# Kernel tuning notes

Measured on AMD Instinct MI355X. Metric: run time of the kernel, lower is better.

The kernel has to match this reference:

```python
import jax, jax.numpy as jnp
import numpy as np

N, B, M, K, C = 120000, 8, 60000, 16, 32
EX = 512  # 128 * expansion_factor 4
EPS = 1e-5


def _bn(h, g, b):
    # BatchNorm1d (training-mode batch stats, biased var), stats over points
    m = h.mean(axis=0)
    v = h.var(axis=0)
    return (h - m) * jax.lax.rsqrt(v + EPS) * g + b


def setup_inputs() -> dict:
    key = jax.random.key(0)
    ks = jax.random.split(key, 20)

    def w(i, shape, fan):
        return jax.random.normal(ks[i], shape, jnp.float32) / np.sqrt(fan)

    inp = {}
    inp["x"] = jax.random.normal(ks[0], (N, C), jnp.float32)
    inp["pos"] = jax.random.normal(ks[1], (N, 3), jnp.float32) * 5.0
    inp["batch"] = jnp.sort(jax.random.randint(ks[2], (N,), 0, B))
    inp["reflectance"] = jax.random.uniform(ks[3], (N,), jnp.float32)
    inp["sf"] = jax.random.uniform(ks[4], (B,), jnp.float32, minval=0.5, maxval=1.5)
    inp["idx"] = jnp.sort(jax.random.randint(ks[5], (M,), 0, N))
    inp["edge_src"] = jax.random.randint(ks[6], (M * K,), 0, N)
    inp["edge_dst"] = jnp.repeat(jnp.arange(M), K)
    # local_nn MLP channels [C+4, 64, 64, 128]; first layer has no BN
    inp["mlp_W1"] = w(7, (C + 4, 64), C + 4); inp["mlp_b1"] = jnp.zeros((64,))
    inp["mlp_W2"] = w(8, (64, 64), 64); inp["mlp_b2"] = jnp.zeros((64,))
    inp["mlp_g2"] = jnp.ones((64,)); inp["mlp_be2"] = jnp.zeros((64,))
    inp["mlp_W3"] = w(9, (64, 128), 64); inp["mlp_b3"] = jnp.zeros((128,))
    inp["mlp_g3"] = jnp.ones((128,)); inp["mlp_be3"] = jnp.zeros((128,))
    # ReflectanceYesNo (1 -> 32 -> 32 -> 1)
    inp["ryn_W1"] = w(10, (1, 32), 1); inp["ryn_b1"] = jnp.zeros((32,))
    inp["ryn_W2"] = w(11, (32, 32), 32); inp["ryn_b2"] = jnp.zeros((32,))
    inp["ryn_W3"] = w(12, (32, 1), 32); inp["ryn_b3"] = jnp.zeros((1,))
    # InvertedResidualBlock 128 -> 512 -> 128 (all 1x1 convs)
    inp["exp_W"] = w(13, (128, EX), 128); inp["exp_b"] = jnp.zeros((EX,))
    inp["exp_g"] = jnp.ones((EX,)); inp["exp_be"] = jnp.zeros((EX,))
    inp["dw_w"] = jax.random.normal(ks[14], (2, EX), jnp.float32)  # depthwise k=1 -> per-channel scale
    inp["dw_b"] = jnp.zeros((2, EX)); inp["dw_g"] = jnp.ones((2, EX)); inp["dw_be"] = jnp.zeros((2, EX))
    inp["pw_W"] = w(15, (2, EX, EX), EX); inp["pw_b"] = jnp.zeros((2, EX))
    inp["pw_g"] = jnp.ones((2, EX)); inp["pw_be"] = jnp.zeros((2, EX))
    inp["c_g"] = jnp.ones((2, EX)); inp["c_be"] = jnp.zeros((2, EX))
    inp["proj_W"] = w(16, (EX, 128), EX); inp["proj_b"] = jnp.zeros((128,))
    inp["proj_g"] = jnp.ones((128,)); inp["proj_be"] = jnp.zeros((128,))
    return inp


def reference(x, pos, batch, reflectance, sf, idx, edge_src, edge_dst,
              mlp_W1, mlp_b1, mlp_W2, mlp_b2, mlp_g2, mlp_be2, mlp_W3, mlp_b3, mlp_g3, mlp_be3,
              ryn_W1, ryn_b1, ryn_W2, ryn_b2, ryn_W3, ryn_b3,
              exp_W, exp_b, exp_g, exp_be, dw_w, dw_b, dw_g, dw_be,
              pw_W, pw_b, pw_g, pw_be, c_g, c_be, proj_W, proj_b, proj_g, proj_be):
    Bn = sf.shape[0]
    Mn = idx.shape[0]
    pos4 = jnp.concatenate([pos[:, :3], reflectance[:, None]], axis=-1)  # [N,4]

    # --- ReflectanceYesNo gating (gumbel_softmax over a size-1 axis == ones, straight-through) ---
    h = jax.nn.relu(reflectance[:, None] @ ryn_W1 + ryn_b1)
    h = jax.nn.relu(h @ ryn_W2 + ryn_b2)
    pooled = jax.ops.segment_sum(h, batch, num_segments=Bn)
    counts = jax.ops.segment_sum(jnp.ones((h.shape[0],), h.dtype), batch, num_segments=Bn)
    logits = (pooled / counts[:, None]) @ ryn_W3 + ryn_b3  # [B,1]
    y_soft = jax.nn.softmax(logits, axis=-1)               # size-1 softmax -> all ones
    y = jax.lax.stop_gradient(jnp.ones_like(y_soft) - y_soft) + y_soft
    gate = jnp.where(jnp.sum(reflectance) != 0.0, y[:, 0][batch], 1.0)
    refl4 = pos4[:, 3] * gate

    # --- scale coords, PointNetConv: gather -> local_nn MLP -> max aggregate ---
    scale = sf[batch][:, None]
    pos_s = jnp.concatenate([pos4[:, :3] / scale, refl4[:, None]], axis=-1)  # [N,4]
    rel = pos_s[edge_src] - pos_s[idx][edge_dst]                              # [E,4]
    msg = jnp.concatenate([x[edge_src], rel], axis=-1)                        # [E,C+4]
    h1 = jax.nn.relu(msg @ mlp_W1 + mlp_b1)
    h2 = _bn(jax.nn.relu(h1 @ mlp_W2 + mlp_b2), mlp_g2, mlp_be2)
    h3 = _bn(jax.nn.relu(h2 @ mlp_W3 + mlp_b3), mlp_g3, mlp_be3)
    agg = jax.ops.segment_max(h3, edge_dst, num_segments=Mn)                  # [M,128]
    agg = jnp.where(jnp.isneginf(agg), 0.0, agg)  # PyG fills isolated nodes with 0

    # --- InvertedResidualBlock (1x1 convs == per-point linears, BN over points) ---
    res = agg
    e = jax.nn.relu(_bn(agg @ exp_W + exp_b, exp_g, exp_be))

    def ds(hh, i):  # DepthwiseSeparableConv1d, k=1
        d = jax.nn.relu(_bn(hh * dw_w[i] + dw_b[i], dw_g[i], dw_be[i]))
        return jax.nn.relu(_bn(d @ pw_W[i] + pw_b[i], pw_g[i], pw_be[i]))

    cmid = jax.nn.relu(_bn(ds(e, 0), c_g[0], c_be[0]))
    cmid = _bn(ds(cmid, 1), c_g[1], c_be[1])
    o = _bn(cmid @ proj_W + proj_b, proj_g, proj_be)
    out = jax.nn.relu(o + res)  # shortcut is identity (in == out channels)

    return (out, pos[idx, :3], batch[idx], reflectance[idx], sf)
```

## Files before the change

### kernel.cpp

```cpp
#include <hip/hip_runtime.h>
#include <hip/hip_bf16.h>
#include <cstdint>

#define DEV_INLINE __device__ __forceinline__

typedef unsigned short u16;
typedef unsigned int   u32;
typedef short bf16x8 __attribute__((ext_vector_type(8)));
typedef float f32x4  __attribute__((ext_vector_type(4)));

constexpr int NP = 120000, NB = 8, NM = 60000, KNN = 16;
constexpr int NE = NM * KNN;
constexpr float EPS = 1e-5f;

constexpr size_t O_POS   = (size_t)NM * 128;
constexpr size_t O_BATCH = O_POS + (size_t)NM * 3;
constexpr size_t O_REFL  = O_BATCH + NM;
constexpr size_t O_SF    = O_REFL + NM;

__device__ float  g_pos_s[(size_t)NP * 4];
__device__ u16    g_xbf[(size_t)NP * 32];
__device__ u16    g_pre2[(size_t)NE * 64];
__device__ u32    g_mm[(size_t)NM * 128];
__device__ float  g_agg[(size_t)NM * 128];
__device__ u16    g_aggbf[(size_t)NM * 128];
__device__ u16    g_bufA[(size_t)NM * 512];
__device__ u16    g_bufB[(size_t)NM * 512];
__device__ float  g_obuf[(size_t)NM * 128];
__device__ float  g_sum[512], g_sqs[512], g_cfa[512], g_cfb[512];
__device__ float  g_b3adj[128], g_pbadj[128];
__device__ u16 g_w1t[64 * 64];
__device__ u16 g_w2t[64 * 64];
__device__ u16 g_w3t[128 * 64];
__device__ u16 g_expwt[512 * 128];
__device__ u16 g_pw0t[512 * 512];
__device__ u16 g_pw1t[512 * 512];
__device__ u16 g_projwt[128 * 512];

template<int ID> DEV_INLINE const u16* ubufsel() {
  if constexpr (ID == 1) return g_aggbf;
  else if constexpr (ID == 2) return g_bufA;
  else return g_bufB;
}
template<int ID> DEV_INLINE u16* obufsel() {
  if constexpr (ID == 2) return g_bufA;
  else return g_bufB;
}
template<int ID> DEV_INLINE const u16* wsel() {
  if constexpr (ID == 3) return g_expwt;
  else if constexpr (ID == 4) return g_pw0t;
  else if constexpr (ID == 5) return g_pw1t;
  else return g_projwt;
}

DEV_INLINE float bf2f(u16 u) { u32 x = (u32)u << 16; float f; __builtin_memcpy(&f, &x, 4); return f; }
DEV_INLINE u16 f2bf(float f) {
  u32 x; __builtin_memcpy(&x, &f, 4);
  return (u16)((x + 0x7FFFu + ((x >> 16) & 1u)) >> 16);
}
DEV_INLINE u32 pack2(float a, float b) { return (u32)f2bf(a) | ((u32)f2bf(b) << 16); }

DEV_INLINE uint4 affine8(uint4 v, int kbase, bool relu) {
  u32 u[4] = {v.x, v.y, v.z, v.w};
  u32 r[4];
#pragma unroll
  for (int q = 0; q < 4; q++) {
    float lo = bf2f((u16)(u[q] & 0xFFFFu));
    float hi = bf2f((u16)(u[q] >> 16));
    lo = fmaf(g_cfa[kbase + 2*q],     lo, g_cfb[kbase + 2*q]);
    hi = fmaf(g_cfa[kbase + 2*q + 1], hi, g_cfb[kbase + 2*q + 1]);
    if (relu) { lo = fmaxf(lo, 0.f); hi = fmaxf(hi, 0.f); }
    r[q] = (u32)f2bf(lo) | ((u32)f2bf(hi) << 16);
  }
  return make_uint4(r[0], r[1], r[2], r[3]);
}

__global__ void prep_pos_x(const float* __restrict__ pos, const int* __restrict__ batch,
                           const float* __restrict__ refl, const float* __restrict__ sf,
                           const float* __restrict__ x) {
  int i = blockIdx.x * blockDim.x + threadIdx.x;
  if (i >= NP) return;
  float s = sf[batch[i]];
  float4 v;
  v.x = pos[(size_t)i*3+0] / s;
  v.y = pos[(size_t)i*3+1] / s;
  v.z = pos[(size_t)i*3+2] / s;
  v.w = refl[i];
  *reinterpret_cast<float4*>(g_pos_s + (size_t)i*4) = v;
  const float4* xr = reinterpret_cast<const float4*>(x + (size_t)i*32);
#pragma unroll
  for (int q = 0; q < 4; q++) {
    float4 a = xr[q*2], b = xr[q*2+1];
    uint4 u = make_uint4(pack2(a.x,a.y), pack2(a.z,a.w), pack2(b.x,b.y), pack2(b.z,b.w));
    *reinterpret_cast<uint4*>(g_xbf + (size_t)i*32 + q*8) = u;
  }
}

__global__ void tail_out(const float* __restrict__ pos, const int* __restrict__ batch,
                         const float* __restrict__ refl, const float* __restrict__ sf,
                         const int* __restrict__ idx, float* __restrict__ out) {
  int i = blockIdx.x * blockDim.x + threadIdx.x;
  if (i < NM) {
    int p = idx[i];
    out[O_POS + (size_t)i*3+0] = pos[(size_t)p*3+0];
    out[O_POS + (size_t)i*3+1] = pos[(size_t)p*3+1];
    out[O_POS + (size_t)i*3+2] = pos[(size_t)p*3+2];
    out[O_BATCH + i] = (float)batch[p];
    out[O_REFL  + i] = refl[p];
  }
  if (i < NB) out[O_SF + i] = sf[i];
}

__global__ void zero_stats() {
  int t = threadIdx.x;
  g_sum[t] = 0.f; g_sqs[t] = 0.f;
}

__global__ void prep_weights(const float* __restrict__ W1, const float* __restrict__ W2,
                             const float* __restrict__ W3, const float* __restrict__ expW,
                             const float* __restrict__ pwW, const float* __restrict__ projW) {
  int i = blockIdx.x * 256 + threadIdx.x;
  const int s0 = 4096, s1 = 4096, s2 = 8192, s3 = 65536, s4 = 262144, s5 = 262144, s6 = 65536;
  if (i < s0) { int n = i >> 6, k = i & 63; g_w1t[i] = (k < 36) ? f2bf(W1[k*64 + n]) : (u16)0; return; }
  i -= s0;
  if (i < s1) { int n = i >> 6, k = i & 63; g_w2t[i] = f2bf(W2[k*64 + n]); return; }
  i -= s1;
  if (i < s2) { int n = i >> 6, k = i & 63; g_w3t[i] = f2bf(W3[k*128 + n]); return; }
  i -= s2;
  if (i < s3) { int n = i >> 7, k = i & 127; g_expwt[i] = f2bf(expW[k*512 + n]); return; }
  i -= s3;
  if (i < s4) { int n = i >> 9, k = i & 511; g_pw0t[i] = f2bf(pwW[k*512 + n]); return; }
  i -= s4;
  if (i < s5) { int n = i >> 9, k = i & 511; g_pw1t[i] = f2bf(pwW[262144 + k*512 + n]); return; }
  i -= s5;
  if (i < s6) { int n = i >> 9, k = i & 511; g_projwt[i] = f2bf(projW[k*128 + n]); return; }
}

__global__ void param_bn(const float* __restrict__ g, const float* __restrict__ be,
                         float n, int C) {
  int c = threadIdx.x;
  if (c < C) {
    float mean = g_sum[c] / n;
    float var  = fmaxf(g_sqs[c] / n - mean * mean, 0.f);
    float a = g[c] * rsqrtf(var + EPS);
    g_cfa[c] = a;
    g_cfb[c] = be[c] - a * mean;
  }
  __syncthreads();
  g_sum[c] = 0.f; g_sqs[c] = 0.f;
}

__global__ void param_dw(const float* __restrict__ w, const float* __restrict__ g,
                         const float* __restrict__ be, float n, int C) {
  int c = threadIdx.x;
  if (c < C) {
    float mean = g_sum[c] / n;
    float var  = fmaxf(g_sqs[c] / n - mean * mean, 0.f);
    float r = rsqrtf(w[c]*w[c]*var + EPS);
    float a = w[c] * r * g[c];
    g_cfa[c] = a;
    g_cfb[c] = be[c] - a * mean;
  }
  __syncthreads();
  g_sum[c] = 0.f; g_sqs[c] = 0.f;
}

template<int SID>
__global__ void scale_fold(const float* __restrict__ bias_in, int N, int K) {
  u16* Wt = (SID == 0) ? g_w3t : g_projwt;
  float* badj = (SID == 0) ? g_b3adj : g_pbadj;
  int w = (blockIdx.x * blockDim.x + threadIdx.x) >> 6;
  int lane = threadIdx.x & 63;
  if (w >= N) return;
  float acc = 0.f;
  for (int k = lane; k < K; k += 64) {
    float wv = bf2f(Wt[(size_t)w*K + k]);
    acc = fmaf(g_cfb[k], wv, acc);
    Wt[(size_t)w*K + k] = f2bf(g_cfa[k] * wv);
  }
#pragma unroll
  for (int o = 32; o; o >>= 1) acc += __shfl_xor(acc, o, 64);
  if (lane == 0) badj[w] = bias_in[w] + acc;
}

constexpr int K1_BLOCKS = 960;
__launch_bounds__(256)
__global__ void k1_edge(const int* __restrict__ esrc, const int* __restrict__ idx,
                        const float* __restrict__ b1v, const float* __restrict__ b2v) {
  __shared__ u16 sH[4][16][72];
  __shared__ float ssum[64], ssqs[64];
  const int tid = threadIdx.x;
  if (tid < 64) { ssum[tid] = 0.f; ssqs[tid] = 0.f; }
  __syncthreads();
  const int w = tid >> 6, lane = tid & 63, l15 = lane & 15, l4 = lane >> 4;
  u16 (*sh)[72] = sH[w];
  bf16x8 w1f[2][4], w2f[2][4];
#pragma unroll
  for (int ks = 0; ks < 2; ks++)
#pragma unroll
    for (int fc = 0; fc < 4; fc++) {
      w1f[ks][fc] = *reinterpret_cast<const bf16x8*>(g_w1t + (size_t)(fc*16+l15)*64 + ks*32 + l4*8);
      w2f[ks][fc] = *reinterpret_cast<const bf16x8*>(g_w2t + (size_t)(fc*16+l15)*64 + ks*32 + l4*8);
    }
  float b1r[4], b2r[4];
#pragma unroll
  for (int fc = 0; fc < 4; fc++) { b1r[fc] = b1v[fc*16+l15]; b2r[fc] = b2v[fc*16+l15]; }
  float s8[4] = {}, q8[4] = {};
  const int t0 = blockIdx.x * 4 + w;
  const int TSTRIDE = K1_BLOCKS * 4;
  int   s_cur = esrc[t0*16 + l15];
  uint4 x_cur = *reinterpret_cast<const uint4*>(g_xbf + (size_t)s_cur*32 + l4*8);
  float4 ps_cur = make_float4(0.f,0.f,0.f,0.f);
  if (l4 == 0) ps_cur = *reinterpret_cast<const float4*>(g_pos_s + (size_t)s_cur*4);
  float4 pc_cur = *reinterpret_cast<const float4*>(g_pos_s + (size_t)idx[t0]*4);

  for (int t = t0; t < NM; t += TSTRIDE) {
    const int tn = t + TSTRIDE;
    int s_nx = 0; uint4 x_nx = make_uint4(0,0,0,0);
    float4 ps_nx = ps_cur, pc_nx = pc_cur;
    if (tn < NM) {
      s_nx = esrc[tn*16 + l15];
      x_nx = *reinterpret_cast<const uint4*>(g_xbf + (size_t)s_nx*32 + l4*8);
      if (l4 == 0) ps_nx = *reinterpret_cast<const float4*>(g_pos_s + (size_t)s_nx*4);
      pc_nx = *reinterpret_cast<const float4*>(g_pos_s + (size_t)idx[tn]*4);
    }
    bf16x8 a0 = __builtin_bit_cast(bf16x8, x_cur);
    uint4 r4 = make_uint4(0,0,0,0);
    if (l4 == 0) {
      r4.x = pack2(ps_cur.x - pc_cur.x, ps_cur.y - pc_cur.y);
      r4.y = pack2(ps_cur.z - pc_cur.z, ps_cur.w - pc_cur.w);
    }
    bf16x8 a1 = __builtin_bit_cast(bf16x8, r4);
    f32x4 acc1[4] = {};
#pragma unroll
    for (int fc = 0; fc < 4; fc++) {
      acc1[fc] = __builtin_amdgcn_mfma_f32_16x16x32_bf16(a0, w1f[0][fc], acc1[fc], 0, 0, 0);
      acc1[fc] = __builtin_amdgcn_mfma_f32_16x16x32_bf16(a1, w1f[1][fc], acc1[fc], 0, 0, 0);
    }
#pragma unroll
    for (int fc = 0; fc < 4; fc++)
#pragma unroll
      for (int r = 0; r < 4; r++)
        sh[l4*4 + r][fc*16 + l15] = f2bf(fmaxf(acc1[fc][r] + b1r[fc], 0.f));
    bf16x8 h0  = *reinterpret_cast<const bf16x8*>(&sh[l15][l4*8]);
    bf16x8 h1v = *reinterpret_cast<const bf16x8*>(&sh[l15][32 + l4*8]);
    f32x4 acc2[4] = {};
#pragma unroll
    for (int fc = 0; fc < 4; fc++) {
      acc2[fc] = __builtin_amdgcn_mfma_f32_16x16x32_bf16(h0,  w2f[0][fc], acc2[fc], 0, 0, 0);
      acc2[fc] = __builtin_amdgcn_mfma_f32_16x16x32_bf16(h1v, w2f[1][fc], acc2[fc], 0, 0, 0);
    }
#pragma unroll
    for (int fc = 0; fc < 4; fc++)
#pragma unroll
      for (int r = 0; r < 4; r++) {
        float v = fmaxf(acc2[fc][r] + b2r[fc], 0.f);
        s8[fc] += v; q8[fc] += v*v;
        sh[l4*4 + r][fc*16 + l15] = f2bf(v);
      }
    uint4 p0 = *reinterpret_cast<const uint4*>(&sh[l15][l4*8]);
    uint4 p1 = *reinterpret_cast<const uint4*>(&sh[l15][32 + l4*8]);
    *reinterpret_cast<uint4*>(g_pre2 + (size_t)t*1024 + lane*8)       = p0;
    *reinterpret_cast<uint4*>(g_pre2 + (size_t)t*1024 + 512 + lane*8) = p1;
    s_cur = s_nx; x_cur = x_nx; ps_cur = ps_nx; pc_cur = pc_nx;
  }
#pragma unroll
  for (int fc = 0; fc < 4; fc++) {
    float sv = s8[fc], qv = q8[fc];
    sv += __shfl_xor(sv, 16, 64); sv += __shfl_xor(sv, 32, 64);
    qv += __shfl_xor(qv, 16, 64); qv += __shfl_xor(qv, 32, 64);
    if (l4 == 0) { atomicAdd(&ssum[fc*16 + l15], sv); atomicAdd(&ssqs[fc*16 + l15], qv); }
  }
  __syncthreads();
  if (tid < 64) { atomicAdd(&g_sum[tid], ssum[tid]); atomicAdd(&g_sqs[tid], ssqs[tid]); }
}

constexpr int K2_BLOCKS = 960;
__launch_bounds__(256)
__global__ void k2_edge() {
  __shared__ float ssum[128], ssqs[128];
  const int tid = threadIdx.x;
  if (tid < 128) { ssum[tid] = 0.f; ssqs[tid] = 0.f; }
  __syncthreads();
  const int lane = tid & 63, l15 = lane & 15, l4 = lane >> 4;
  const int wglobal = blockIdx.x * 4 + (tid >> 6);
  const int WSTRIDE = K2_BLOCKS * 4;
  bf16x8 w3f[2][8];
#pragma unroll
  for (int ks = 0; ks < 2; ks++)
#pragma unroll
    for (int fc = 0; fc < 8; fc++)
      w3f[ks][fc] = *reinterpret_cast<const bf16x8*>(g_w3t + (size_t)(fc*16 + l15)*64 + ks*32 + l4*8);
  float bv[8];
#pragma unroll
  for (int fc = 0; fc < 8; fc++) bv[fc] = g_b3adj[fc*16 + l15];
  float s[8] = {}, q[8] = {};
  int t = wglobal;
  uint4 an0 = make_uint4(0,0,0,0), an1 = an0;
  if (t < NM) {
    const uint4* p = reinterpret_cast<const uint4*>(g_pre2 + (size_t)t*1024 + lane*8);
    an0 = p[0]; an1 = p[64];
  }
  for (; t < NM; t += WSTRIDE) {
    uint4 a0 = an0, a1 = an1;
    int tn = t + WSTRIDE;
    if (tn < NM) {
      const uint4* p = reinterpret_cast<const uint4*>(g_pre2 + (size_t)tn*1024 + lane*8);
      an0 = p[0]; an1 = p[64];
    }
    bf16x8 af0 = __builtin_bit_cast(bf16x8, a0);
    bf16x8 af1 = __builtin_bit_cast(bf16x8, a1);
    f32x4 acc[8] = {};
#pragma unroll
    for (int fc = 0; fc < 8; fc++) {
      acc[fc] = __builtin_amdgcn_mfma_f32_16x16x32_bf16(af0, w3f[0][fc], acc[fc], 0, 0, 0);
      acc[fc] = __builtin_amdgcn_mfma_f32_16x16x32_bf16(af1, w3f[1][fc], acc[fc], 0, 0, 0);
    }
    u32 rbase = (u32)t * 128u;
#pragma unroll
    for (int fc = 0; fc < 8; fc++) {
      float v0 = fmaxf(acc[fc][0] + bv[fc], 0.f);
      float v1 = fmaxf(acc[fc][1] + bv[fc], 0.f);
      float v2 = fmaxf(acc[fc][2] + bv[fc], 0.f);
      float v3 = fmaxf(acc[fc][3] + bv[fc], 0.f);
      s[fc] += (v0 + v1) + (v2 + v3);
      q[fc] += (v0*v0 + v1*v1) + (v2*v2 + v3*v3);
      float mx = fmaxf(fmaxf(v0, v1), fmaxf(v2, v3));
      float mn = fminf(fminf(v0, v1), fminf(v2, v3));
      mx = fmaxf(mx, __shfl_xor(mx, 16, 64)); mx = fmaxf(mx, __shfl_xor(mx, 32, 64));
      mn = fminf(mn, __shfl_xor(mn, 16, 64)); mn = fminf(mn, __shfl_xor(mn, 32, 64));
      if (l4 == (fc & 3))
        g_mm[rbase + fc*16 + l15] = (u32)f2bf(mx) | ((u32)f2bf(mn) << 16);
    }
  }
#pragma unroll
  for (int fc = 0; fc < 8; fc++) {
    float sv = s[fc], qv = q[fc];
    sv += __shfl_xor(sv, 16, 64); sv += __shfl_xor(sv, 32, 64);
    qv += __shfl_xor(qv, 16, 64); qv += __shfl_xor(qv, 32, 64);
    if (l4 == 0) { atomicAdd(&ssum[fc*16 + l15], sv); atomicAdd(&ssqs[fc*16 + l15], qv); }
  }
  __syncthreads();
  if (tid < 128) { atomicAdd(&g_sum[tid], ssum[tid]); atomicAdd(&g_sqs[tid], ssqs[tid]); }
}

__global__ void k3_agg() {
  int i4 = (blockIdx.x * 256 + threadIdx.x) * 4;
  if (i4 >= NM * 128) return;
  int c = i4 & 127;
  uint4 mm = *reinterpret_cast<const uint4*>(g_mm + i4);
  float4 a = *reinterpret_cast<const float4*>(g_cfa + c);
  float4 b = *reinterpret_cast<const float4*>(g_cfb + c);
  u32 u[4] = {mm.x, mm.y, mm.z, mm.w};
  float av[4] = {a.x, a.y, a.z, a.w};
  float bb[4] = {b.x, b.y, b.z, b.w};
  float4 r;
  float* rr = &r.x;
#pragma unroll
  for (int j = 0; j < 4; j++) {
    float mx = bf2f((u16)(u[j] & 0xFFFFu));
    float mn = bf2f((u16)(u[j] >> 16));
    rr[j] = av[j] > 0.f ? fmaf(av[j], mx, bb[j]) : fmaf(av[j], mn, bb[j]);
  }
  *reinterpret_cast<float4*>(g_agg + i4) = r;
  uint2 pk; pk.x = pack2(r.x, r.y); pk.y = pack2(r.z, r.w);
  *reinterpret_cast<uint2*>(g_aggbf + i4) = pk;
}

template<int AID, int WID, int OID, bool PRO_AFF, bool PRO_RELU, bool OUT_BF16, bool BIAS_DEV>
__launch_bounds__(256)
__global__ void gemm_mfma(const float* __restrict__ bias, int Mrows, int Ncols, int Kdim) {
  const u16* __restrict__ A  = ubufsel<AID>();
  const u16* __restrict__ Bt = wsel<WID>();
  __shared__ u16 As[128][40];
  __shared__ u16 Bs[128][40];
  __shared__ float ssum[128], ssqs[128];
  const int tid = threadIdx.x;
  const int m0 = blockIdx.x * 128, n0 = blockIdx.y * 128;
  if (tid < 128) { ssum[tid] = 0.f; ssqs[tid] = 0.f; }
  const int wave = tid >> 6, lane = tid & 63, l15 = lane & 15, l4 = lane >> 4;
  const int wr = wave >> 1, wc = wave & 1;
  const int srow = tid >> 1, sseg = tid & 1;
  const int gr = m0 + srow;
  const bool aval = gr < Mrows;
  f32x4 acc[4][4] = {};
  for (int k0 = 0; k0 < Kdim; k0 += 32) {
    uint4 va0 = make_uint4(0,0,0,0), va1 = va0;
    if (aval) {
      const uint4* p = reinterpret_cast<const uint4*>(A + (size_t)gr*Kdim + k0 + sseg*16);
      va0 = p[0]; va1 = p[1];
    }
    if (PRO_AFF) {
      va0 = affine8(va0, k0 + sseg*16,     PRO_RELU);
      va1 = affine8(va1, k0 + sseg*16 + 8, PRO_RELU);
    }
    const uint4* pb = reinterpret_cast<const uint4*>(Bt + (size_t)(n0 + srow)*Kdim + k0 + sseg*16);
    uint4 vb0 = pb[0], vb1 = pb[1];
    __syncthreads();
    *reinterpret_cast<uint4*>(&As[srow][sseg*16])     = va0;
    *reinterpret_cast<uint4*>(&As[srow][sseg*16 + 8]) = va1;
    *reinterpret_cast<uint4*>(&Bs[srow][sseg*16])     = vb0;
    *reinterpret_cast<uint4*>(&Bs[srow][sseg*16 + 8]) = vb1;
    __syncthreads();
    bf16x8 af[4], bf[4];
#pragma unroll
    for (int fr = 0; fr < 4; fr++)
      af[fr] = *reinterpret_cast<const bf16x8*>(&As[wr*64 + fr*16 + l15][l4*8]);
#pragma unroll
    for (int fc = 0; fc < 4; fc++)
      bf[fc] = *reinterpret_cast<const bf16x8*>(&Bs[wc*64 + fc*16 + l15][l4*8]);
#pragma unroll
    for (int fr = 0; fr < 4; fr++)
#pragma unroll
      for (int fc = 0; fc < 4; fc++)
        acc[fr][fc] = __builtin_amdgcn_mfma_f32_16x16x32_bf16(af[fr], bf[fc], acc[fr][fc], 0, 0, 0);
  }
  const int orow = m0 + wr*64 + l4*4;
#pragma unroll
  for (int fc = 0; fc < 4; fc++) {
    int col = n0 + wc*64 + fc*16 + l15;
    float bvv = BIAS_DEV ? g_pbadj[col] : bias[col];
    float s = 0.f, q = 0.f;
#pragma unroll
    for (int fr = 0; fr < 4; fr++)
#pragma unroll
      for (int r = 0; r < 4; r++) {
        int row = orow + fr*16 + r;
        if (row < Mrows) {
          float v = acc[fr][fc][r] + bvv;
          s += v; q += v*v;
          if (OUT_BF16) obufsel<OID>()[(size_t)row*Ncols + col] = f2bf(v);
          else          g_obuf[(size_t)row*Ncols + col] = v;
        }
      }
    atomicAdd(&ssum[wc*64 + fc*16 + l15], s);
    atomicAdd(&ssqs[wc*64 + fc*16 + l15], q);
  }
  __syncthreads();
  if (tid < 128) { atomicAdd(&g_sum[n0 + tid], ssum[tid]); atomicAdd(&g_sqs[n0 + tid], ssqs[tid]); }
}

template<int INID, int OUTID>
__launch_bounds__(256)
__global__ void ew_stats(int rows) {
  const u16* __restrict__ X = ubufsel<INID>();
  u16* __restrict__ Y = obufsel<OUTID>();
  __shared__ float ssum[512], ssqs[512];
  const int tid = threadIdx.x;
  ssum[tid] = 0.f; ssum[tid+256] = 0.f; ssqs[tid] = 0.f; ssqs[tid+256] = 0.f;
  __syncthreads();
  const int c0 = (tid & 63) * 8;
  const int rl = tid >> 6;
  float a[8], b[8];
#pragma unroll
  for (int j = 0; j < 8; j++) { a[j] = g_cfa[c0+j]; b[j] = g_cfb[c0+j]; }
  float s[8] = {}, q[8] = {};
  for (int r = blockIdx.x*4 + rl; r < rows; r += gridDim.x*4) {
    uint4 v = *reinterpret_cast<const uint4*>(X + (size_t)r*512 + c0);
    u32 u[4] = {v.x, v.y, v.z, v.w}, o[4];
#pragma unroll
    for (int t = 0; t < 4; t++) {
      float lo = bf2f((u16)(u[t] & 0xFFFFu));
      float hi = bf2f((u16)(u[t] >> 16));
      lo = fmaxf(fmaf(a[2*t],   lo, b[2*t]),   0.f);
      hi = fmaxf(fmaf(a[2*t+1], hi, b[2*t+1]), 0.f);
      s[2*t] += lo; q[2*t] += lo*lo; s[2*t+1] += hi; q[2*t+1] += hi*hi;
      o[t] = (u32)f2bf(lo) | ((u32)f2bf(hi) << 16);
    }
    *reinterpret_cast<uint4*>(Y + (size_t)r*512 + c0) = make_uint4(o[0], o[1], o[2], o[3]);
  }
#pragma unroll
  for (int j = 0; j < 8; j++) { atomicAdd(&ssum[c0+j], s[j]); atomicAdd(&ssqs[c0+j], q[j]); }
  __syncthreads();
  atomicAdd(&g_sum[tid],     ssum[tid]);     atomicAdd(&g_sqs[tid],     ssqs[tid]);
  atomicAdd(&g_sum[tid+256], ssum[tid+256]); atomicAdd(&g_sqs[tid+256], ssqs[tid+256]);
}

__global__ void final_out(float* __restrict__ out) {
  int i4 = (blockIdx.x * 256 + threadIdx.x) * 4;
  if (i4 >= NM * 128) return;
  int c = i4 & 127;
  float4 o  = *reinterpret_cast<const float4*>(g_obuf + i4);
  float4 ag = *reinterpret_cast<const float4*>(g_agg + i4);
  float4 a  = *reinterpret_cast<const float4*>(g_cfa + c);
  float4 b  = *reinterpret_cast<const float4*>(g_cfb + c);
  float4 r;
  r.x = fmaxf(fmaf(a.x, o.x, b.x) + ag.x, 0.f);
  r.y = fmaxf(fmaf(a.y, o.y, b.y) + ag.y, 0.f);
  r.z = fmaxf(fmaf(a.z, o.z, b.z) + ag.z, 0.f);
  r.w = fmaxf(fmaf(a.w, o.w, b.w) + ag.w, 0.f);
  *reinterpret_cast<float4*>(out + i4) = r;
}

extern "C" void kernel_launch(void* const* d_in, const int* in_sizes, int n_in,
                              void* d_out, int out_size, void* d_ws, size_t ws_size,
                              hipStream_t stream) {
  const float* x     = (const float*)d_in[0];
  const float* pos   = (const float*)d_in[1];
  const int*   batch = (const int*)  d_in[2];
  const float* refl  = (const float*)d_in[3];
  const float* sf    = (const float*)d_in[4];
  const int*   idx   = (const int*)  d_in[5];
  const int*   esrc  = (const int*)  d_in[6];
  const float* W1  = (const float*)d_in[8];
  const float* b1  = (const float*)d_in[9];
  const float* W2  = (const float*)d_in[10];
  const float* b2  = (const float*)d_in[11];
  const float* g2  = (const float*)d_in[12];
  const float* be2 = (const float*)d_in[13];
  const float* W3  = (const float*)d_in[14];
  const float* b3  = (const float*)d_in[15];
  const float* g3  = (const float*)d_in[16];
  const float* be3 = (const float*)d_in[17];
  const float* expW  = (const float*)d_in[24];
  const float* expb  = (const float*)d_in[25];
  const float* expg  = (const float*)d_in[26];
  const float* expbe = (const float*)d_in[27];
  const float* dww  = (const float*)d_in[28];
  const float* dwg  = (const float*)d_in[30];
  const float* dwbe = (const float*)d_in[31];
  const float* pwW  = (const float*)d_in[32];
  const float* pwb  = (const float*)d_in[33];
  const float* pwg  = (const float*)d_in[34];
  const float* pwbe = (const float*)d_in[35];
  const float* cg   = (const float*)d_in[36];
  const float* cbe  = (const float*)d_in[37];
  const float* projW  = (const float*)d_in[38];
  const float* projb  = (const float*)d_in[39];
  const float* projg  = (const float*)d_in[40];
  const float* projbe = (const float*)d_in[41];
  float* out = (float*)d_out;

  const float fNE = (float)NE, fNM = (float)NM;

  prep_weights<<<2624, 256, 0, stream>>>(W1, W2, W3, expW, pwW, projW);
  prep_pos_x<<<(NP + 255)/256, 256, 0, stream>>>(pos, batch, refl, sf, x);
  tail_out<<<(NM + 255)/256, 256, 0, stream>>>(pos, batch, refl, sf, idx, out);
  zero_stats<<<1, 512, 0, stream>>>();

  k1_edge<<<K1_BLOCKS, 256, 0, stream>>>(esrc, idx, b1, b2);
  param_bn<<<1, 512, 0, stream>>>(g2, be2, fNE, 64);
  scale_fold<0><<<32, 256, 0, stream>>>(b3, 128, 64);
  k2_edge<<<K2_BLOCKS, 256, 0, stream>>>();
  param_bn<<<1, 512, 0, stream>>>(g3, be3, fNE, 128);
  k3_agg<<<NM*128/1024, 256, 0, stream>>>();

  gemm_mfma<1, 3, 2, false, false, true, false><<<dim3(469, 4), 256, 0, stream>>>(expb, NM, 512, 128);
  param_bn<<<1, 512, 0, stream>>>(expg, expbe, fNM, 512);
  ew_stats<2, 2><<<512, 256, 0, stream>>>(NM);
  param_dw<<<1, 512, 0, stream>>>(dww, dwg, dwbe, fNM, 512);
  gemm_mfma<2, 4, 3, true, true, true, false><<<dim3(469, 4), 256, 0, stream>>>(pwb, NM, 512, 512);
  param_bn<<<1, 512, 0, stream>>>(pwg, pwbe, fNM, 512);
  ew_stats<3, 3><<<512, 256, 0, stream>>>(NM);
  param_bn<<<1, 512, 0, stream>>>(cg, cbe, fNM, 512);
  ew_stats<3, 3><<<512, 256, 0, stream>>>(NM);
  param_dw<<<1, 512, 0, stream>>>(dww + 512, dwg + 512, dwbe + 512, fNM, 512);
  gemm_mfma<3, 5, 2, true, true, true, false><<<dim3(469, 4), 256, 0, stream>>>(pwb + 512, NM, 512, 512);
  param_bn<<<1, 512, 0, stream>>>(pwg + 512, pwbe + 512, fNM, 512);
  ew_stats<2, 2><<<512, 256, 0, stream>>>(NM);
  param_bn<<<1, 512, 0, stream>>>(cg + 512, cbe + 512, fNM, 512);
  scale_fold<1><<<32, 256, 0, stream>>>(projb, 128, 512);
  gemm_mfma<2, 6, 0, false, false, false, true><<<dim3(469, 1), 256, 0, stream>>>(projb, NM, 128, 512);
  param_bn<<<1, 512, 0, stream>>>(projg, projbe, fNM, 128);
  final_out<<<NM*128/1024, 256, 0, stream>>>(out);
}
```

Before: 812.2 us.

## Double-buffer LDS tiles in MFMA GEMM and prefetch next K-tile during compute

The GEMM main loop now uses two LDS buffers. It issues the global loads for the next K-tile before running the MFMAs on the current one, so memory latency overlaps with compute and each iteration needs one barrier instead of two. The prologue affine coefficients are loaded as float4 vectors alongside the data, not read per element. Launch bounds request 3 blocks per CU, and the extra registers for prefetched data plus doubled LDS may limit occupancy.

```diff
diff --git a/kernel.cpp b/kernel.cpp
--- a/kernel.cpp
+++ b/kernel.cpp
@@ -60,6 +60,22 @@
 }
 DEV_INLINE u32 pack2(float a, float b) { return (u32)f2bf(a) | ((u32)f2bf(b) << 16); }
 
+DEV_INLINE uint4 affine8r(uint4 v, float4 A0, float4 A1, float4 B0, float4 B1, bool relu) {
+  float av[8] = {A0.x,A0.y,A0.z,A0.w,A1.x,A1.y,A1.z,A1.w};
+  float bv[8] = {B0.x,B0.y,B0.z,B0.w,B1.x,B1.y,B1.z,B1.w};
+  u32 u[4] = {v.x, v.y, v.z, v.w}, r[4];
+#pragma unroll
+  for (int q = 0; q < 4; q++) {
+    float lo = bf2f((u16)(u[q] & 0xFFFFu));
+    float hi = bf2f((u16)(u[q] >> 16));
+    lo = fmaf(av[2*q],   lo, bv[2*q]);
+    hi = fmaf(av[2*q+1], hi, bv[2*q+1]);
+    if (relu) { lo = fmaxf(lo, 0.f); hi = fmaxf(hi, 0.f); }
+    r[q] = (u32)f2bf(lo) | ((u32)f2bf(hi) << 16);
+  }
+  return make_uint4(r[0], r[1], r[2], r[3]);
+}
+
 DEV_INLINE uint4 affine8(uint4 v, int kbase, bool relu) {
   u32 u[4] = {v.x, v.y, v.z, v.w};
   u32 r[4];
@@ -368,12 +384,12 @@
 }
 
 template<int AID, int WID, int OID, bool PRO_AFF, bool PRO_RELU, bool OUT_BF16, bool BIAS_DEV>
-__launch_bounds__(256)
+__launch_bounds__(256, 3)
 __global__ void gemm_mfma(const float* __restrict__ bias, int Mrows, int Ncols, int Kdim) {
   const u16* __restrict__ A  = ubufsel<AID>();
   const u16* __restrict__ Bt = wsel<WID>();
-  __shared__ u16 As[128][40];
-  __shared__ u16 Bs[128][40];
+  __shared__ u16 As[2][128][40];
+  __shared__ u16 Bs[2][128][40];
   __shared__ float ssum[128], ssqs[128];
   const int tid = threadIdx.x;
   const int m0 = blockIdx.x * 128, n0 = blockIdx.y * 128;
@@ -383,38 +399,75 @@
   const int srow = tid >> 1, sseg = tid & 1;
   const int gr = m0 + srow;
   const bool aval = gr < Mrows;
+  const size_t aoff = (size_t)gr * Kdim + sseg * 16;
+  const size_t boff = (size_t)(n0 + srow) * Kdim + sseg * 16;
   f32x4 acc[4][4] = {};
-  for (int k0 = 0; k0 < Kdim; k0 += 32) {
-    uint4 va0 = make_uint4(0,0,0,0), va1 = va0;
+  const int nt = Kdim >> 5;
+
+  uint4 va0, va1, vb0, vb1;
+  float4 ca0, ca1, ca2, ca3, cb0, cb1, cb2, cb3;
+
+  auto LOAD = [&](int t) {
+    const int k0 = t * 32;
+    va0 = make_uint4(0,0,0,0); va1 = va0;
     if (aval) {
-      const uint4* p = reinterpret_cast<const uint4*>(A + (size_t)gr*Kdim + k0 + sseg*16);
+      const uint4* p = reinterpret_cast<const uint4*>(A + aoff + k0);
       va0 = p[0]; va1 = p[1];
     }
+    const uint4* pb = reinterpret_cast<const uint4*>(Bt + boff + k0);
+    vb0 = pb[0]; vb1 = pb[1];
     if (PRO_AFF) {
-      va0 = affine8(va0, k0 + sseg*16,     PRO_RELU);
-      va1 = affine8(va1, k0 + sseg*16 + 8, PRO_RELU);
-    }
-    const uint4* pb = reinterpret_cast<const uint4*>(Bt + (size_t)(n0 + srow)*Kdim + k0 + sseg*16);
-    uint4 vb0 = pb[0], vb1 = pb[1];
-    __syncthreads();
-    *reinterpret_cast<uint4*>(&As[srow][sseg*16])     = va0;
-    *reinterpret_cast<uint4*>(&As[srow][sseg*16 + 8]) = va1;
-    *reinterpret_cast<uint4*>(&Bs[srow][sseg*16])     = vb0;
-    *reinterpret_cast<uint4*>(&Bs[srow][sseg*16 + 8]) = vb1;
-    __syncthreads();
+      const int kb = k0 + sseg * 16;
+      ca0 = *reinterpret_cast<const float4*>(g_cfa + kb);
+      ca1 = *reinterpret_cast<const float4*>(g_cfa + kb + 4);
+      ca2 = *reinterpret_cast<const float4*>(g_cfa + kb + 8);
+      ca3 = *reinterpret_cast<const float4*>(g_cfa + kb + 12);
+      cb0 = *reinterpret_cast<const float4*>(g_cfb + kb);
+      cb1 = *reinterpret_cast<const float4*>(g_cfb + kb + 4);
+      cb2 = *reinterpret_cast<const float4*>(g_cfb + kb + 8);
+      cb3 = *reinterpret_cast<const float4*>(g_cfb + kb + 12);
+    }
+  };
+  auto WRITE = [&](int buf) {
+    uint4 wa0 = va0, wa1 = va1;
+    if (PRO_AFF) {
+      wa0 = affine8r(va0, ca0, ca1, cb0, cb1, PRO_RELU);
+      wa1 = affine8r(va1, ca2, ca3, cb2, cb3, PRO_RELU);
+    }
+    *reinterpret_cast<uint4*>(&As[buf][srow][sseg*16])     = wa0;
+    *reinterpret_cast<uint4*>(&As[buf][srow][sseg*16 + 8]) = wa1;
+    *reinterpret_cast<uint4*>(&Bs[buf][srow][sseg*16])     = vb0;
+    *reinterpret_cast<uint4*>(&Bs[buf][srow][sseg*16 + 8]) = vb1;
+  };
+  auto MFMA = [&](int buf) {
     bf16x8 af[4], bf[4];
 #pragma unroll
     for (int fr = 0; fr < 4; fr++)
-      af[fr] = *reinterpret_cast<const bf16x8*>(&As[wr*64 + fr*16 + l15][l4*8]);
+      af[fr] = *reinterpret_cast<const bf16x8*>(&As[buf][wr*64 + fr*16 + l15][l4*8]);
 #pragma unroll
     for (int fc = 0; fc < 4; fc++)
-      bf[fc] = *reinterpret_cast<const bf16x8*>(&Bs[wc*64 + fc*16 + l15][l4*8]);
+      bf[fc] = *reinterpret_cast<const bf16x8*>(&Bs[buf][wc*64 + fc*16 + l15][l4*8]);
 #pragma unroll
     for (int fr = 0; fr < 4; fr++)
 #pragma unroll
       for (int fc = 0; fc < 4; fc++)
         acc[fr][fc] = __builtin_amdgcn_mfma_f32_16x16x32_bf16(af[fr], bf[fc], acc[fr][fc], 0, 0, 0);
-  }
+  };
+
+  LOAD(0);
+  WRITE(0);
+  __syncthreads();
+  int cur = 0;
+  for (int t = 0; ; ) {
+    const bool more = (t + 1 < nt);
+    if (more) LOAD(t + 1);
+    MFMA(cur);
+    if (!more) break;
+    WRITE(cur ^ 1);
+    __syncthreads();
+    cur ^= 1; ++t;
+  }
+
   const int orow = m0 + wr*64 + l4*4;
 #pragma unroll
   for (int fc = 0; fc < 4; fc++) {
```

New measurement: 804.8 us. Within noise of the previous version (-0.9%).

## Double-buffer MFMA GEMM with direct global-to-LDS loads and split affine prologue

Applied to the files above, without the earlier changes.

The bf16 MFMA GEMM now stages A and B tiles with `global_load_lds` into double-buffered, unpadded LDS. The next K-tile's load overlaps the current tile's MFMAs, which removes one barrier per iteration and the register round-trip. Because direct-to-LDS loads cannot transform data, the BN-affine+ReLU prologue moves into a separate `ew_apply` pass over the 60000x512 activation before each pointwise GEMM. That pass adds an extra full read/write of the activation. Other changes: a 1D grid with N-panels adjacent for A reuse in cache, launch bounds of 3 blocks per CU, and doubled `ew_stats` grids. The last M tile now loads rows past 60000 without a bound check, and the unpadded LDS rows may cause bank conflicts.

```diff
diff --git a/kernel.cpp b/kernel.cpp
--- a/kernel.cpp
+++ b/kernel.cpp
@@ -8,6 +8,9 @@
 typedef unsigned int   u32;
 typedef short bf16x8 __attribute__((ext_vector_type(8)));
 typedef float f32x4  __attribute__((ext_vector_type(4)));
+
+#define AS_GLOBAL(p) ((const __attribute__((address_space(1))) void*)(p))
+#define AS_LDS(p)    ((__attribute__((address_space(3))) void*)(p))
 
 constexpr int NP = 120000, NB = 8, NM = 60000, KNN = 16;
 constexpr int NE = NM * KNN;
@@ -60,21 +63,6 @@
 }
 DEV_INLINE u32 pack2(float a, float b) { return (u32)f2bf(a) | ((u32)f2bf(b) << 16); }
 
-DEV_INLINE uint4 affine8(uint4 v, int kbase, bool relu) {
-  u32 u[4] = {v.x, v.y, v.z, v.w};
-  u32 r[4];
-#pragma unroll
-  for (int q = 0; q < 4; q++) {
-    float lo = bf2f((u16)(u[q] & 0xFFFFu));
-    float hi = bf2f((u16)(u[q] >> 16));
-    lo = fmaf(g_cfa[kbase + 2*q],     lo, g_cfb[kbase + 2*q]);
-    hi = fmaf(g_cfa[kbase + 2*q + 1], hi, g_cfb[kbase + 2*q + 1]);
-    if (relu) { lo = fmaxf(lo, 0.f); hi = fmaxf(hi, 0.f); }
-    r[q] = (u32)f2bf(lo) | ((u32)f2bf(hi) << 16);
-  }
-  return make_uint4(r[0], r[1], r[2], r[3]);
-}
-
 __global__ void prep_pos_x(const float* __restrict__ pos, const int* __restrict__ batch,
                            const float* __restrict__ refl, const float* __restrict__ sf,
                            const float* __restrict__ x) {
@@ -367,54 +355,58 @@
   *reinterpret_cast<uint2*>(g_aggbf + i4) = pk;
 }
 
-template<int AID, int WID, int OID, bool PRO_AFF, bool PRO_RELU, bool OUT_BF16, bool BIAS_DEV>
-__launch_bounds__(256)
-__global__ void gemm_mfma(const float* __restrict__ bias, int Mrows, int Ncols, int Kdim) {
+template<int AID, int WID, int OID, int NPAN, bool OUT_BF16, bool BIAS_DEV>
+__launch_bounds__(256, 3)
+__global__ void gemm_mfma(const float* __restrict__ bias, int Mrows, int Kdim) {
+  const int Ncols = NPAN * 128;
   const u16* __restrict__ A  = ubufsel<AID>();
   const u16* __restrict__ Bt = wsel<WID>();
-  __shared__ u16 As[128][40];
-  __shared__ u16 Bs[128][40];
+  __shared__ u16 As[2][128][32];
+  __shared__ u16 Bs[2][128][32];
   __shared__ float ssum[128], ssqs[128];
   const int tid = threadIdx.x;
-  const int m0 = blockIdx.x * 128, n0 = blockIdx.y * 128;
+  const int bid = blockIdx.x;
+  const int m0 = (bid / NPAN) * 128, n0 = (bid % NPAN) * 128;
   if (tid < 128) { ssum[tid] = 0.f; ssqs[tid] = 0.f; }
   const int wave = tid >> 6, lane = tid & 63, l15 = lane & 15, l4 = lane >> 4;
   const int wr = wave >> 1, wc = wave & 1;
-  const int srow = tid >> 1, sseg = tid & 1;
-  const int gr = m0 + srow;
-  const bool aval = gr < Mrows;
+  const int ckk = (lane & 3) * 8;
   f32x4 acc[4][4] = {};
-  for (int k0 = 0; k0 < Kdim; k0 += 32) {
-    uint4 va0 = make_uint4(0,0,0,0), va1 = va0;
-    if (aval) {
-      const uint4* p = reinterpret_cast<const uint4*>(A + (size_t)gr*Kdim + k0 + sseg*16);
-      va0 = p[0]; va1 = p[1];
-    }
-    if (PRO_AFF) {
-      va0 = affine8(va0, k0 + sseg*16,     PRO_RELU);
-      va1 = affine8(va1, k0 + sseg*16 + 8, PRO_RELU);
-    }
-    const uint4* pb = reinterpret_cast<const uint4*>(Bt + (size_t)(n0 + srow)*Kdim + k0 + sseg*16);
-    uint4 vb0 = pb[0], vb1 = pb[1];
-    __syncthreads();
-    *reinterpret_cast<uint4*>(&As[srow][sseg*16])     = va0;
-    *reinterpret_cast<uint4*>(&As[srow][sseg*16 + 8]) = va1;
-    *reinterpret_cast<uint4*>(&Bs[srow][sseg*16])     = vb0;
-    *reinterpret_cast<uint4*>(&Bs[srow][sseg*16 + 8]) = vb1;
-    __syncthreads();
+  const int nt = Kdim >> 5;
+
+  auto STAGE = [&](int buf, int t) {
+    const int k0 = t * 32;
+#pragma unroll
+    for (int i = 0; i < 2; i++) {
+      const int c = wave * 2 + i;
+      const int row = c * 16 + (lane >> 2);
+      const u16* ga = A  + (size_t)(m0 + row) * Kdim + k0 + ckk;
+      const u16* gb = Bt + (size_t)(n0 + row) * Kdim + k0 + ckk;
+      __builtin_amdgcn_global_load_lds(AS_GLOBAL(ga), AS_LDS(&As[buf][c*16][0]), 16, 0, 0);
+      __builtin_amdgcn_global_load_lds(AS_GLOBAL(gb), AS_LDS(&Bs[buf][c*16][0]), 16, 0, 0);
+    }
+  };
+
+  STAGE(0, 0);
+  __syncthreads();
+  int cur = 0;
+  for (int t = 0; t < nt; ++t) {
+    if (t + 1 < nt) STAGE(cur ^ 1, t + 1);
     bf16x8 af[4], bf[4];
 #pragma unroll
     for (int fr = 0; fr < 4; fr++)
-      af[fr] = *reinterpret_cast<const bf16x8*>(&As[wr*64 + fr*16 + l15][l4*8]);
+      af[fr] = *reinterpret_cast<const bf16x8*>(&As[cur][wr*64 + fr*16 + l15][l4*8]);
 #pragma unroll
     for (int fc = 0; fc < 4; fc++)
-      bf[fc] = *reinterpret_cast<const bf16x8*>(&Bs[wc*64 + fc*16 + l15][l4*8]);
+      bf[fc] = *reinterpret_cast<const bf16x8*>(&Bs[cur][wc*64 + fc*16 + l15][l4*8]);
 #pragma unroll
     for (int fr = 0; fr < 4; fr++)
 #pragma unroll
       for (int fc = 0; fc < 4; fc++)
         acc[fr][fc] = __builtin_amdgcn_mfma_f32_16x16x32_bf16(af[fr], bf[fc], acc[fr][fc], 0, 0, 0);
-  }
+    if (t + 1 < nt) { __syncthreads(); cur ^= 1; }
+  }
+
   const int orow = m0 + wr*64 + l4*4;
 #pragma unroll
   for (int fc = 0; fc < 4; fc++) {
@@ -474,6 +466,32 @@
   __syncthreads();
   atomicAdd(&g_sum[tid],     ssum[tid]);     atomicAdd(&g_sqs[tid],     ssqs[tid]);
   atomicAdd(&g_sum[tid+256], ssum[tid+256]); atomicAdd(&g_sqs[tid+256], ssqs[tid+256]);
+}
+
+template<int INID, int OUTID>
+__launch_bounds__(256)
+__global__ void ew_apply(int rows) {
+  const u16* __restrict__ X = ubufsel<INID>();
+  u16* __restrict__ Y = obufsel<OUTID>();
+  const int tid = threadIdx.x;
+  const int c0 = (tid & 63) * 8;
+  const int rl = tid >> 6;
+  float a[8], b[8];
+#pragma unroll
+  for (int j = 0; j < 8; j++) { a[j] = g_cfa[c0+j]; b[j] = g_cfb[c0+j]; }
+  for (int r = blockIdx.x*4 + rl; r < rows; r += gridDim.x*4) {
+    uint4 v = *reinterpret_cast<const uint4*>(X + (size_t)r*512 + c0);
+    u32 u[4] = {v.x, v.y, v.z, v.w}, o[4];
+#pragma unroll
+    for (int t = 0; t < 4; t++) {
+      float lo = bf2f((u16)(u[t] & 0xFFFFu));
+      float hi = bf2f((u16)(u[t] >> 16));
+      lo = fmaxf(fmaf(a[2*t],   lo, b[2*t]),   0.f);
+      hi = fmaxf(fmaf(a[2*t+1], hi, b[2*t+1]), 0.f);
+      o[t] = (u32)f2bf(lo) | ((u32)f2bf(hi) << 16);
+    }
+    *reinterpret_cast<uint4*>(Y + (size_t)r*512 + c0) = make_uint4(o[0], o[1], o[2], o[3]);
+  }
 }
 
 __global__ void final_out(float* __restrict__ out) {
@@ -545,22 +563,24 @@
   param_bn<<<1, 512, 0, stream>>>(g3, be3, fNE, 128);
   k3_agg<<<NM*128/1024, 256, 0, stream>>>();
 
-  gemm_mfma<1, 3, 2, false, false, true, false><<<dim3(469, 4), 256, 0, stream>>>(expb, NM, 512, 128);
+  gemm_mfma<1, 3, 2, 4, true, false><<<469*4, 256, 0, stream>>>(expb, NM, 128);
   param_bn<<<1, 512, 0, stream>>>(expg, expbe, fNM, 512);
-  ew_stats<2, 2><<<512, 256, 0, stream>>>(NM);
+  ew_stats<2, 2><<<1024, 256, 0, stream>>>(NM);
   param_dw<<<1, 512, 0, stream>>>(dww, dwg, dwbe, fNM, 512);
-  gemm_mfma<2, 4, 3, true, true, true, false><<<dim3(469, 4), 256, 0, stream>>>(pwb, NM, 512, 512);
+  ew_apply<2, 3><<<1024, 256, 0, stream>>>(NM);
+  gemm_mfma<3, 4, 2, 4, true, false><<<469*4, 256, 0, stream>>>(pwb, NM, 512);
   param_bn<<<1, 512, 0, stream>>>(pwg, pwbe, fNM, 512);
-  ew_stats<3, 3><<<512, 256, 0, stream>>>(NM);
+  ew_stats<2, 2><<<1024, 256, 0, stream>>>(NM);
   param_bn<<<1, 512, 0, stream>>>(cg, cbe, fNM, 512);
-  ew_stats<3, 3><<<512, 256, 0, stream>>>(NM);
+  ew_stats<2, 2><<<1024, 256, 0, stream>>>(NM);
   param_dw<<<1, 512, 0, stream>>>(dww + 512, dwg + 512, dwbe + 512, fNM, 512);
-  gemm_mfma<3, 5, 2, true, true, true, false><<<dim3(469, 4), 256, 0, stream>>>(pwb + 512, NM, 512, 512);
+  ew_apply<2, 3><<<1024, 256, 0, stream>>>(NM);
+  gemm_mfma<3, 5, 2, 4, true, false><<<469*4, 256, 0, stream>>>(pwb + 512, NM, 512);
   param_bn<<<1, 512, 0, stream>>>(pwg + 512, pwbe + 512, fNM, 512);
-  ew_stats<2, 2><<<512, 256, 0, stream>>>(NM);
+  ew_stats<2, 2><<<1024, 256, 0, stream>>>(NM);
   param_bn<<<1, 512, 0, stream>>>(cg + 512, cbe + 512, fNM, 512);
   scale_fold<1><<<32, 256, 0, stream>>>(projb, 128, 512);
-  gemm_mfma<2, 6, 0, false, false, false, true><<<dim3(469, 1), 256, 0, stream>>>(projb, NM, 128, 512);
+  gemm_mfma<2, 6, 0, 1, false, true><<<469, 256, 0, stream>>>(projb, NM, 512);
   param_bn<<<1, 512, 0, stream>>>(projg, projbe, fNM, 128);
   final_out<<<NM*128/1024, 256, 0, stream>>>(out);
 }
```

Result: no change. 828.0 us (+1.9%).
